# Optimization experiments

Measured on AMD Instinct MI355X. Metric: run time of the kernel, lower is better.

The kernel has to match this reference:

```python
import jax, jax.numpy as jnp
import numpy as np

B, S, E, H = 8, 1024, 1024, 16
D = E // H          # head_dim = 64
FF = 4 * E          # mlp hidden = 4096
EPS = 1e-5


def setup_inputs() -> dict:
    key = jax.random.key(0)
    ks = jax.random.split(key, 12)
    s_e = 1.0 / np.sqrt(E)
    s_ff = 1.0 / np.sqrt(FF)
    return {
        "x": jax.random.normal(ks[0], (B, S, E), jnp.float32),
        # per-head q/k/v projections stacked: [H, E, D] (math layout: y = x @ W + b)
        "Wq": jax.random.normal(ks[1], (H, E, D), jnp.float32) * s_e,
        "bq": jnp.zeros((H, D), jnp.float32),
        "Wk": jax.random.normal(ks[2], (H, E, D), jnp.float32) * s_e,
        "bk": jnp.zeros((H, D), jnp.float32),
        "Wv": jax.random.normal(ks[3], (H, E, D), jnp.float32) * s_e,
        "bv": jnp.zeros((H, D), jnp.float32),
        # output projection [E, E]
        "Wo": jax.random.normal(ks[4], (E, E), jnp.float32) * s_e,
        "bo": jnp.zeros((E,), jnp.float32),
        # layernorms
        "g1": jnp.ones((E,), jnp.float32),
        "beta1": jnp.zeros((E,), jnp.float32),
        "g2": jnp.ones((E,), jnp.float32),
        "beta2": jnp.zeros((E,), jnp.float32),
        # MLP
        "W1": jax.random.normal(ks[5], (E, FF), jnp.float32) * s_e,
        "c1": jnp.zeros((FF,), jnp.float32),
        "W2": jax.random.normal(ks[6], (FF, E), jnp.float32) * s_ff,
        "c2": jnp.zeros((E,), jnp.float32),
    }


def _layernorm(x, g, b):
    mu = jnp.mean(x, axis=-1, keepdims=True)
    var = jnp.mean(jnp.square(x - mu), axis=-1, keepdims=True)
    return (x - mu) * jax.lax.rsqrt(var + EPS) * g + b


def _block(x, Wq, bq, Wk, bk, Wv, bv, Wo, bo, g1, beta1, g2, beta2, W1, c1, W2, c2):
    # --- attention sublayer (pre-norm) ---
    xn = _layernorm(x, g1, beta1)
    # all heads at once (equivalent to the per-head Python loop)
    q = jnp.einsum("bse,hed->bhsd", xn, Wq) + bq[:, None, :]
    k = jnp.einsum("bse,hed->bhsd", xn, Wk) + bk[:, None, :]
    v = jnp.einsum("bse,hed->bhsd", xn, Wv) + bv[:, None, :]
    scale = D ** -0.5
    scores = jnp.einsum("bhsd,bhtd->bhst", q, k) * scale  # [B,H,S,S]
    w = jax.nn.softmax(scores, axis=-1)
    ctx = jnp.einsum("bhst,bhtd->bhsd", w, v)             # [B,H,S,D]
    ctx = ctx.transpose(0, 2, 1, 3).reshape(x.shape[0], x.shape[1], E)  # concat heads
    attn_out = ctx @ Wo + bo
    x = x + attn_out
    # --- MLP sublayer (pre-norm) ---
    xn = _layernorm(x, g2, beta2)
    h = jax.nn.gelu(xn @ W1 + c1, approximate=False)
    return x + (h @ W2 + c2)


def reference(x, Wq, bq, Wk, bk, Wv, bv, Wo, bo, g1, beta1, g2, beta2, W1, c1, W2, c2):
    return _block(x, Wq, bq, Wk, bk, Wv, bv, Wo, bo, g1, beta1, g2, beta2, W1, c1, W2, c2)
```

## Files before the change

kernel.cpp:

```cpp
#include <hip/hip_runtime.h>
#include <math.h>


typedef _Float16 h16;
typedef __attribute__((ext_vector_type(8))) _Float16 f16x8;
typedef __attribute__((ext_vector_type(4))) float f32x4;

__device__ __forceinline__ void gl2lds16(const void* g, void* l) {
  __builtin_amdgcn_global_load_lds(
      (const __attribute__((address_space(1))) void*)g,
      (__attribute__((address_space(3))) void*)l, 16, 0, 0);
}

__global__ __launch_bounds__(256) void repack_kernel(
    const float* __restrict__ Wq, const float* __restrict__ Wk,
    const float* __restrict__ Wv, const float* __restrict__ Wo,
    const float* __restrict__ W1, const float* __restrict__ W2,
    const float* __restrict__ bq, const float* __restrict__ bk,
    const float* __restrict__ bv,
    h16* __restrict__ WqkvT, h16* __restrict__ WoT, h16* __restrict__ W1T,
    h16* __restrict__ W2T, float* __restrict__ bqkv)
{
  const int t = blockIdx.x;
  const int tid = threadIdx.x;
  if (t == 3072) {
    for (int i = tid; i < 3072; i += 256)
      bqkv[i] = (i < 1024) ? bq[i] : (i < 2048 ? bk[i - 1024] : bv[i - 2048]);
    return;
  }
  __shared__ float ld[64 * 65];

  const float* src; h16* dst;
  int sRS, dRS, k0, sn0, dn0;
  if (t < 768) {
    const int m = t >> 8, tt = t & 255, h = tt >> 4, tk = tt & 15;
    src = ((m == 0) ? Wq : (m == 1) ? Wk : Wv) + (size_t)h * 65536;
    dst = WqkvT; sRS = 64; dRS = 1024;
    k0 = tk * 64; sn0 = 0; dn0 = m * 1024 + h * 64;
  } else if (t < 1024) {
    const int tt = t - 768, tk = tt >> 4, tn = tt & 15;
    src = Wo; dst = WoT; sRS = 1024; dRS = 1024;
    k0 = tk * 64; sn0 = tn * 64; dn0 = tn * 64;
  } else if (t < 2048) {
    const int tt = t - 1024, tk = tt >> 6, tn = tt & 63;
    src = W1; dst = W1T; sRS = 4096; dRS = 1024;
    k0 = tk * 64; sn0 = tn * 64; dn0 = tn * 64;
  } else {
    const int tt = t - 2048, tk = tt >> 4, tn = tt & 15;
    src = W2; dst = W2T; sRS = 1024; dRS = 4096;
    k0 = tk * 64; sn0 = tn * 64; dn0 = tn * 64;
  }

  #pragma unroll
  for (int p = 0; p < 16; ++p) {
    const int idx = p * 256 + tid;
    const int r = idx >> 6, c = idx & 63;
    ld[c * 65 + r] = src[(size_t)(k0 + r) * sRS + sn0 + c];
  }
  __syncthreads();
  #pragma unroll
  for (int p = 0; p < 8; ++p) {
    const int idx = p * 512 + tid * 2;
    const int n = idx >> 6, k = idx & 63;
    union { unsigned int u; h16 e[2]; } pk;
    pk.e[0] = (h16)ld[n * 65 + k];
    pk.e[1] = (h16)ld[n * 65 + k + 1];
    *(unsigned int*)&dst[(size_t)(dn0 + n) * dRS + k0 + k] = pk.u;
  }
}

template <int IT>
__global__ __launch_bounds__(256) void ln_kernel(
    const void* __restrict__ in, const float* __restrict__ gw,
    const float* __restrict__ bw, h16* __restrict__ outp)
{
  const int row = blockIdx.x;
  const int tid = threadIdx.x;
  float v[4];
  if (IT == 0) {
    const float* p = (const float*)in + (size_t)row * 1024 + tid * 4;
    float4 tt = *(const float4*)p;
    v[0] = tt.x; v[1] = tt.y; v[2] = tt.z; v[3] = tt.w;
  } else {
    const h16* p = (const h16*)in + (size_t)row * 1024 + tid * 4;
    union { uint2 u; h16 h[4]; } raw;
    raw.u = *(const uint2*)p;
    v[0] = (float)raw.h[0]; v[1] = (float)raw.h[1];
    v[2] = (float)raw.h[2]; v[3] = (float)raw.h[3];
  }
  float s = v[0] + v[1] + v[2] + v[3];
  float ss = v[0]*v[0] + v[1]*v[1] + v[2]*v[2] + v[3]*v[3];
  #pragma unroll
  for (int off = 32; off >= 1; off >>= 1) {
    s += __shfl_down(s, off);
    ss += __shfl_down(ss, off);
  }
  __shared__ float red[8];
  const int w = tid >> 6;
  if ((tid & 63) == 0) { red[w] = s; red[4 + w] = ss; }
  __syncthreads();
  s = red[0] + red[1] + red[2] + red[3];
  ss = red[4] + red[5] + red[6] + red[7];
  const float mean = s * (1.0f / 1024.0f);
  const float var = ss * (1.0f / 1024.0f) - mean * mean;
  const float inv = rsqrtf(fmaxf(var, 0.0f) + 1e-5f);
  union { uint2 u; h16 h[4]; } pk;
  #pragma unroll
  for (int i = 0; i < 4; ++i)
    pk.h[i] = (h16)((v[i] - mean) * inv * gw[tid * 4 + i] + bw[tid * 4 + i]);
  *(uint2*)(outp + (size_t)row * 1024 + tid * 4) = pk.u;
}

#define GEMM8_LDS 131072

template <int MODE>
__global__ __launch_bounds__(512, 2) void gemm8_bt(
    const h16* __restrict__ A, const h16* __restrict__ BT,
    const float* __restrict__ bias, const void* __restrict__ res,
    void* __restrict__ out, int M, int N, int K)
{
  extern __shared__ __align__(16) char smem[];
  const int tid = threadIdx.x;
  const int lane = tid & 63;
  const int l15 = lane & 15, quad = lane >> 4;
  const int w = tid >> 6;
  const int wr = w >> 2, wc = w & 3;
  const int m0 = blockIdx.y * 256, n0 = blockIdx.x * 256;
  const int NT = K >> 5;

  const int sk = (((tid & 3) ^ ((tid >> 3) & 3)) << 3);
  const h16* gA = A + (size_t)(m0 + (tid >> 2)) * K + sk;
  const h16* gB = BT + (size_t)(n0 + (tid >> 2)) * K + sk;
  const int d0 = tid * 16;

  const int x4 = (quad ^ ((l15 >> 1) & 3)) << 4;
  const int aoff = (wr * 128 + l15) * 64 + x4;
  const int boff = 16384 + (wc * 64 + l15) * 64 + x4;

  f32x4 zero = {0.f, 0.f, 0.f, 0.f};
  f32x4 acc[8][4];
  #pragma unroll
  for (int a = 0; a < 8; ++a)
    #pragma unroll
    for (int b = 0; b < 4; ++b) acc[a][b] = zero;

  #pragma unroll
  for (int tt = 0; tt < 3; ++tt) {
    char* bp = smem + tt * 32768;
    gl2lds16(gA + (size_t)tt * 32, bp + d0);
    gl2lds16(gA + (size_t)tt * 32 + (size_t)128 * K, bp + 8192 + d0);
    gl2lds16(gB + (size_t)tt * 32, bp + 16384 + d0);
    gl2lds16(gB + (size_t)tt * 32 + (size_t)128 * K, bp + 24576 + d0);
  }
  asm volatile("s_waitcnt vmcnt(8)" ::: "memory");
  __builtin_amdgcn_sched_barrier(0);
  __builtin_amdgcn_s_barrier();

  for (int t = 0; t < NT; ++t) {
    const char* Tb = smem + (t & 3) * 32768;
    char* Pb = smem + ((t + 3) & 3) * 32768;
    const bool pf = (t + 3) < NT;
    f16x8 bf[4], af[4], af2[4];

    #pragma unroll
    for (int ni = 0; ni < 4; ++ni)
      bf[ni] = *(const f16x8*)(Tb + boff + ni * 1024);
    #pragma unroll
    for (int mi = 0; mi < 4; ++mi)
      af[mi] = *(const f16x8*)(Tb + aoff + mi * 1024);
    if (pf) {
      const h16* g = gA + (size_t)(t + 3) * 32;
      gl2lds16(g, Pb + d0);
      gl2lds16(g + (size_t)128 * K, Pb + 8192 + d0);
    }
    __builtin_amdgcn_s_barrier();
    __builtin_amdgcn_s_setprio(1);
    #pragma unroll
    for (int mi = 0; mi < 4; ++mi)
      #pragma unroll
      for (int ni = 0; ni < 4; ++ni)
        acc[mi][ni] = __builtin_amdgcn_mfma_f32_16x16x32_f16(af[mi], bf[ni], acc[mi][ni], 0, 0, 0);
    __builtin_amdgcn_s_setprio(0);

    #pragma unroll
    for (int mi = 0; mi < 4; ++mi)
      af2[mi] = *(const f16x8*)(Tb + aoff + (mi + 4) * 1024);
    if (pf) {
      const h16* g = gB + (size_t)(t + 3) * 32;
      gl2lds16(g, Pb + 16384 + d0);
      gl2lds16(g + (size_t)128 * K, Pb + 24576 + d0);
    }
    __builtin_amdgcn_s_barrier();
    __builtin_amdgcn_s_setprio(1);
    #pragma unroll
    for (int mi = 0; mi < 4; ++mi)
      #pragma unroll
      for (int ni = 0; ni < 4; ++ni)
        acc[mi + 4][ni] = __builtin_amdgcn_mfma_f32_16x16x32_f16(af2[mi], bf[ni], acc[mi + 4][ni], 0, 0, 0);
    __builtin_amdgcn_s_setprio(0);

    if (pf) {
      asm volatile("s_waitcnt vmcnt(8)" ::: "memory");
    } else if (t + 3 == NT) {
      asm volatile("s_waitcnt vmcnt(4)" ::: "memory");
    } else if (t + 2 == NT) {
      asm volatile("s_waitcnt vmcnt(0)" ::: "memory");
    }
    __builtin_amdgcn_sched_barrier(0);
    __builtin_amdgcn_s_barrier();
  }

  #pragma unroll
  for (int mi = 0; mi < 8; ++mi) {
    #pragma unroll
    for (int ni = 0; ni < 4; ++ni) {
      #pragma unroll
      for (int i = 0; i < 4; ++i) {
        const int r = m0 + wr * 128 + mi * 16 + quad * 4 + i;
        const int c = n0 + wc * 64 + ni * 16 + l15;
        const size_t idx = (size_t)r * N + c;
        float v = acc[mi][ni][i] + bias[c];
        if (MODE == 0) {
          ((h16*)out)[idx] = (h16)v;
        } else if (MODE == 1) {
          v += ((const float*)res)[idx];
          ((h16*)out)[idx] = (h16)v;
        } else if (MODE == 2) {
          const float e = __expf(v * (-1.5957691216f - 0.0713548163f * v * v));
          v = v / (1.0f + e);
          ((h16*)out)[idx] = (h16)v;
        } else {
          v += (float)((const h16*)res)[idx];
          ((float*)out)[idx] = v;
        }
      }
    }
  }
}

#define GEMM_LDS 147456

template <int MODE>
__global__ __launch_bounds__(512, 2) void gemm_bt(
    const h16* __restrict__ A, const h16* __restrict__ BT,
    const float* __restrict__ bias, const void* __restrict__ res,
    void* __restrict__ out, int M, int N, int K)
{
  extern __shared__ __align__(16) char smem[];
  const int tid = threadIdx.x;
  const int lane = tid & 63, w = tid >> 6;
  const int l15 = lane & 15, quad = lane >> 4;
  const int wm = w >> 1, wn = w & 1;
  const int m0 = blockIdx.y * 256, n0 = blockIdx.x * 128;
  const int NT = K >> 6;

  const int srow = w * 8 + (lane >> 3);
  const int scol = ((lane & 7) ^ ((lane >> 3) & 7)) * 8;
  const h16* gA = A + (size_t)(m0 + srow) * K + scol;
  const h16* gB = BT + (size_t)(n0 + srow) * K + scol;
  const int ldsw = w * 1024;

  const int arow = wm * 64 + l15;
  const int brow = wn * 64 + l15;
  const int x7 = l15 & 7;
  const int sw0 = (quad ^ x7) << 4;
  const int sw1 = ((4 | quad) ^ x7) << 4;

  f32x4 zero = {0.f, 0.f, 0.f, 0.f};
  f32x4 acc[4][4];
  #pragma unroll
  for (int a = 0; a < 4; ++a)
    #pragma unroll
    for (int b = 0; b < 4; ++b) acc[a][b] = zero;

  {
    char* b0 = smem;
    char* b1 = smem + 49152;
    #pragma unroll
    for (int j = 0; j < 4; ++j) gl2lds16(gA + (size_t)j * 64 * K, b0 + j * 8192 + ldsw);
    #pragma unroll
    for (int j = 0; j < 2; ++j) gl2lds16(gB + (size_t)j * 64 * K, b0 + 32768 + j * 8192 + ldsw);
    #pragma unroll
    for (int j = 0; j < 4; ++j) gl2lds16(gA + 64 + (size_t)j * 64 * K, b1 + j * 8192 + ldsw);
    #pragma unroll
    for (int j = 0; j < 2; ++j) gl2lds16(gB + 64 + (size_t)j * 64 * K, b1 + 32768 + j * 8192 + ldsw);
  }
  asm volatile("s_waitcnt vmcnt(6)" ::: "memory");
  __builtin_amdgcn_sched_barrier(0);
  __builtin_amdgcn_s_barrier();

  int cur = 0, pre = 2;
  for (int t = 0; t < NT; ++t) {
    const char* Ab = smem + cur * 49152;
    const char* Bb = Ab + 32768;
    char* Pb = smem + pre * 49152;
    const bool pf = (t + 2) < NT;
    f16x8 af[4], bf[4][2];

    #pragma unroll
    for (int mi = 0; mi < 4; ++mi) {
      af[mi] = *(const f16x8*)(Ab + (arow + mi * 16) * 128 + sw0);
    }
    f16x8 af1[4];
    #pragma unroll
    for (int mi = 0; mi < 4; ++mi)
      af1[mi] = *(const f16x8*)(Ab + (arow + mi * 16) * 128 + sw1);
    #pragma unroll
    for (int ni = 0; ni < 2; ++ni) {
      bf[ni][0] = *(const f16x8*)(Bb + (brow + ni * 16) * 128 + sw0);
      bf[ni][1] = *(const f16x8*)(Bb + (brow + ni * 16) * 128 + sw1);
    }
    if (pf) {
      const h16* g = gA + (size_t)(t + 2) * 64;
      #pragma unroll
      for (int j = 0; j < 4; ++j) gl2lds16(g + (size_t)j * 64 * K, Pb + j * 8192 + ldsw);
    }
    __builtin_amdgcn_s_barrier();
    __builtin_amdgcn_s_setprio(1);
    #pragma unroll
    for (int mi = 0; mi < 4; ++mi)
      #pragma unroll
      for (int ni = 0; ni < 2; ++ni) {
        acc[mi][ni] = __builtin_amdgcn_mfma_f32_16x16x32_f16(af[mi], bf[ni][0], acc[mi][ni], 0, 0, 0);
        acc[mi][ni] = __builtin_amdgcn_mfma_f32_16x16x32_f16(af1[mi], bf[ni][1], acc[mi][ni], 0, 0, 0);
      }
    __builtin_amdgcn_s_setprio(0);
    __builtin_amdgcn_s_barrier();

    #pragma unroll
    for (int ni = 2; ni < 4; ++ni) {
      bf[ni][0] = *(const f16x8*)(Bb + (brow + ni * 16) * 128 + sw0);
      bf[ni][1] = *(const f16x8*)(Bb + (brow + ni * 16) * 128 + sw1);
    }
    if (pf) {
      const h16* g = gB + (size_t)(t + 2) * 64;
      #pragma unroll
      for (int j = 0; j < 2; ++j) gl2lds16(g + (size_t)j * 64 * K, Pb + 32768 + j * 8192 + ldsw);
    }
    __builtin_amdgcn_s_barrier();
    __builtin_amdgcn_s_setprio(1);
    #pragma unroll
    for (int mi = 0; mi < 4; ++mi)
      #pragma unroll
      for (int ni = 2; ni < 4; ++ni) {
        acc[mi][ni] = __builtin_amdgcn_mfma_f32_16x16x32_f16(af[mi], bf[ni][0], acc[mi][ni], 0, 0, 0);
        acc[mi][ni] = __builtin_amdgcn_mfma_f32_16x16x32_f16(af1[mi], bf[ni][1], acc[mi][ni], 0, 0, 0);
      }
    __builtin_amdgcn_s_setprio(0);
    if (pf) {
      asm volatile("s_waitcnt vmcnt(6)" ::: "memory");
    } else if (t + 2 == NT) {
      asm volatile("s_waitcnt vmcnt(0)" ::: "memory");
    }
    __builtin_amdgcn_sched_barrier(0);
    __builtin_amdgcn_s_barrier();
    cur = (cur == 2) ? 0 : cur + 1;
    pre = (pre == 2) ? 0 : pre + 1;
  }

  #pragma unroll
  for (int mi = 0; mi < 4; ++mi) {
    #pragma unroll
    for (int ni = 0; ni < 4; ++ni) {
      #pragma unroll
      for (int i = 0; i < 4; ++i) {
        const int r = m0 + wm * 64 + mi * 16 + quad * 4 + i;
        const int c = n0 + wn * 64 + ni * 16 + l15;
        const size_t idx = (size_t)r * N + c;
        float v = acc[mi][ni][i] + bias[c];
        if (MODE == 0) {
          ((h16*)out)[idx] = (h16)v;
        } else if (MODE == 1) {
          v += ((const float*)res)[idx];
          ((h16*)out)[idx] = (h16)v;
        } else if (MODE == 2) {
          const float e = __expf(v * (-1.5957691216f - 0.0713548163f * v * v));
          v = v / (1.0f + e);
          ((h16*)out)[idx] = (h16)v;
        } else {
          v += (float)((const h16*)res)[idx];
          ((float*)out)[idx] = v;
        }
      }
    }
  }
}

__global__ __launch_bounds__(256, 2) void attn_kernel(
    const h16* __restrict__ qkv, h16* __restrict__ ctx)
{
  const int qb = blockIdx.x;
  const int bh = blockIdx.y;
  const int b = bh >> 4, h = bh & 15;
  const int tid = threadIdx.x;
  const int w = tid >> 6, lane = tid & 63;
  const int l15 = lane & 15, quad = lane >> 4;

  __shared__ __align__(16) h16 Ks[64 * 80];
  __shared__ __align__(16) h16 Vt[64 * 80];
  __shared__ __align__(16) h16 Ps[256 * 80];

  const size_t qrow0 = (size_t)(b * 1024 + qb * 256);
  for (int c = tid; c < 2048; c += 256) {
    const int row = c >> 3, kc = (c & 7) * 8;
    uint4 raw = *(const uint4*)(qkv + (qrow0 + row) * 3072 + h * 64 + kc);
    union { uint4 v; h16 e[8]; } in4, out4;
    in4.v = raw;
    #pragma unroll
    for (int i = 0; i < 8; ++i) out4.e[i] = in4.e[i] * (h16)0.125f;
    *(uint4*)&Ps[row * 80 + kc] = out4.v;
  }
  __syncthreads();
  f16x8 aq[4][2];
  #pragma unroll
  for (int r = 0; r < 4; ++r)
    #pragma unroll
    for (int s = 0; s < 2; ++s)
      aq[r][s] = *(const f16x8*)&Ps[(w * 64 + r * 16 + l15) * 80 + s * 32 + quad * 8];

  f32x4 zero = {0.f, 0.f, 0.f, 0.f};
  f32x4 o_acc[4][4];
  float l_p[4][4];
  #pragma unroll
  for (int r = 0; r < 4; ++r)
    #pragma unroll
    for (int i = 0; i < 4; ++i) { o_acc[r][i] = zero; l_p[r][i] = 0.f; }

  h16* Pw = &Ps[w * 64 * 80];

  for (int jt = 0; jt < 16; ++jt) {
    __syncthreads();
    const size_t kv0 = (size_t)(b * 1024 + jt * 64);
    for (int c = tid; c < 512; c += 256) {
      const int row = c >> 3, kc = (c & 7) * 8;
      *(uint4*)&Ks[row * 80 + kc] =
          *(const uint4*)(qkv + (kv0 + row) * 3072 + 1024 + h * 64 + kc);
    }
    #pragma unroll
    for (int cc = 0; cc < 2; ++cc) {
      const int d0 = (w + cc * 4) * 8;
      uint4 raw = *(const uint4*)(qkv + (kv0 + lane) * 3072 + 2048 + h * 64 + d0);
      union { uint4 v; h16 e[8]; } in4;
      in4.v = raw;
      #pragma unroll
      for (int i = 0; i < 8; ++i) Vt[(d0 + i) * 80 + lane] = in4.e[i];
    }
    __syncthreads();

    f16x8 kf[4][2];
    #pragma unroll
    for (int ni = 0; ni < 4; ++ni)
      #pragma unroll
      for (int s = 0; s < 2; ++s)
        kf[ni][s] = *(const f16x8*)&Ks[(ni * 16 + l15) * 80 + s * 32 + quad * 8];
    #pragma unroll
    for (int r = 0; r < 4; ++r) {
      f32x4 s_acc[4];
      #pragma unroll
      for (int i = 0; i < 4; ++i) s_acc[i] = zero;
      #pragma unroll
      for (int ni = 0; ni < 4; ++ni)
        #pragma unroll
        for (int s = 0; s < 2; ++s)
          s_acc[ni] = __builtin_amdgcn_mfma_f32_16x16x32_f16(aq[r][s], kf[ni][s], s_acc[ni], 0, 0, 0);
      #pragma unroll
      for (int ni = 0; ni < 4; ++ni)
        #pragma unroll
        for (int i = 0; i < 4; ++i) {
          float p = __expf(s_acc[ni][i]);
          l_p[r][i] += p;
          Pw[(r * 16 + quad * 4 + i) * 80 + ni * 16 + l15] = (h16)p;
        }
    }

    f16x8 vf[4][2];
    #pragma unroll
    for (int ni = 0; ni < 4; ++ni)
      #pragma unroll
      for (int s = 0; s < 2; ++s)
        vf[ni][s] = *(const f16x8*)&Vt[(ni * 16 + l15) * 80 + s * 32 + quad * 8];
    #pragma unroll
    for (int r = 0; r < 4; ++r) {
      f16x8 ap0 = *(const f16x8*)&Pw[(r * 16 + l15) * 80 + quad * 8];
      f16x8 ap1 = *(const f16x8*)&Pw[(r * 16 + l15) * 80 + 32 + quad * 8];
      #pragma unroll
      for (int ni = 0; ni < 4; ++ni) {
        o_acc[r][ni] = __builtin_amdgcn_mfma_f32_16x16x32_f16(ap0, vf[ni][0], o_acc[r][ni], 0, 0, 0);
        o_acc[r][ni] = __builtin_amdgcn_mfma_f32_16x16x32_f16(ap1, vf[ni][1], o_acc[r][ni], 0, 0, 0);
      }
    }
  }

  #pragma unroll
  for (int r = 0; r < 4; ++r)
    #pragma unroll
    for (int i = 0; i < 4; ++i) {
      float lt = l_p[r][i];
      #pragma unroll
      for (int off = 1; off < 16; off <<= 1) lt += __shfl_xor(lt, off);
      const float rinv = 1.0f / lt;
      const size_t row = qrow0 + w * 64 + r * 16 + quad * 4 + i;
      #pragma unroll
      for (int ni = 0; ni < 4; ++ni)
        ctx[row * 1024 + h * 64 + ni * 16 + l15] = (h16)(o_acc[r][ni][i] * rinv);
    }
}

extern "C" void kernel_launch(void* const* d_in, const int* in_sizes, int n_in,
                              void* d_out, int out_size, void* d_ws, size_t ws_size,
                              hipStream_t stream) {
  const float* x   = (const float*)d_in[0];
  const float* Wq  = (const float*)d_in[1];
  const float* bq  = (const float*)d_in[2];
  const float* Wk  = (const float*)d_in[3];
  const float* bk  = (const float*)d_in[4];
  const float* Wv  = (const float*)d_in[5];
  const float* bv  = (const float*)d_in[6];
  const float* Wo  = (const float*)d_in[7];
  const float* bo  = (const float*)d_in[8];
  const float* g1  = (const float*)d_in[9];
  const float* be1 = (const float*)d_in[10];
  const float* g2  = (const float*)d_in[11];
  const float* be2 = (const float*)d_in[12];
  const float* W1  = (const float*)d_in[13];
  const float* c1  = (const float*)d_in[14];
  const float* W2  = (const float*)d_in[15];
  const float* c2  = (const float*)d_in[16];

  char* ws = (char*)d_ws;
  h16*   WqkvT = (h16*)(ws + 0);
  h16*   WoT   = (h16*)(ws + 6291456);
  h16*   W1T   = (h16*)(ws + 8388608);
  h16*   W2T   = (h16*)(ws + 16777216);
  float* bqkv  = (float*)(ws + 25165824);
  h16*   bufA  = (h16*)(ws + 25178112);
  h16*   qkv   = (h16*)(ws + 41955328);
  h16*   x1    = (h16*)(ws + 41955328);
  h16*   hbuf  = (h16*)(ws + 58732544);

  static bool attr_done = false;
  if (!attr_done) {
    hipFuncSetAttribute((const void*)gemm_bt<1>, hipFuncAttributeMaxDynamicSharedMemorySize, GEMM_LDS);
    hipFuncSetAttribute((const void*)gemm_bt<3>, hipFuncAttributeMaxDynamicSharedMemorySize, GEMM_LDS);
    hipFuncSetAttribute((const void*)gemm8_bt<0>, hipFuncAttributeMaxDynamicSharedMemorySize, GEMM8_LDS);
    hipFuncSetAttribute((const void*)gemm8_bt<2>, hipFuncAttributeMaxDynamicSharedMemorySize, GEMM8_LDS);
    attr_done = true;
  }

  repack_kernel<<<dim3(3073), dim3(256), 0, stream>>>(Wq, Wk, Wv, Wo, W1, W2, bq, bk, bv,
                                                      WqkvT, WoT, W1T, W2T, bqkv);
  ln_kernel<0><<<dim3(8192), dim3(256), 0, stream>>>(x, g1, be1, bufA);
  gemm8_bt<0><<<dim3(12, 32), dim3(512), GEMM8_LDS, stream>>>(bufA, WqkvT, bqkv, nullptr, qkv,
                                                              8192, 3072, 1024);
  attn_kernel<<<dim3(4, 128), dim3(256), 0, stream>>>(qkv, bufA);
  gemm_bt<1><<<dim3(8, 32), dim3(512), GEMM_LDS, stream>>>(bufA, WoT, bo, x, x1,
                                                           8192, 1024, 1024);
  ln_kernel<1><<<dim3(8192), dim3(256), 0, stream>>>(x1, g2, be2, bufA);
  gemm8_bt<2><<<dim3(16, 32), dim3(512), GEMM8_LDS, stream>>>(bufA, W1T, c1, nullptr, hbuf,
                                                              8192, 4096, 1024);
  gemm_bt<3><<<dim3(8, 32), dim3(512), GEMM_LDS, stream>>>(hbuf, W2T, c2, x1, d_out,
                                                           8192, 1024, 4096);
}
```

Measured before the change: 506.8 us.

## Rewrite 256x256 GEMM mainloop as double-buffered K=64 ping-pong with quadrant MFMA phases

Replaces the 4-stage K=32 pipeline in the QKV and W1 GEMMs with two 64 KB LDS buffers holding K=64 tiles, an 8-way XOR swizzle, and a hand-scheduled loop. Each K=64 tile is processed in four quadrant MFMA phases. Each phase is wrapped in barriers and interleaved with partial global-to-LDS stages of the next tile. The aim is to keep LDS reads and global prefetch hidden behind MFMA work and to reduce per-iteration waitcnt and barrier overhead per K element. In exchange there are more barriers per tile, shallower prefetch depth, and reliance on exact vmcnt counts that must be correct.

```diff
diff --git a/kernel.cpp b/kernel.cpp
--- a/kernel.cpp
+++ b/kernel.cpp
@@ -111,31 +111,34 @@
   *(uint2*)(outp + (size_t)row * 1024 + tid * 4) = pk.u;
 }
 
-#define GEMM8_LDS 131072
+#define GEMM201_LDS 131072
 
 template <int MODE>
-__global__ __launch_bounds__(512, 2) void gemm8_bt(
+__global__ __launch_bounds__(512, 2) void gemm201(
     const h16* __restrict__ A, const h16* __restrict__ BT,
     const float* __restrict__ bias, const void* __restrict__ res,
     void* __restrict__ out, int M, int N, int K)
 {
   extern __shared__ __align__(16) char smem[];
   const int tid = threadIdx.x;
-  const int lane = tid & 63;
+  const int lane = tid & 63, w = tid >> 6;
   const int l15 = lane & 15, quad = lane >> 4;
-  const int w = tid >> 6;
   const int wr = w >> 2, wc = w & 3;
   const int m0 = blockIdx.y * 256, n0 = blockIdx.x * 256;
-  const int NT = K >> 5;
-
-  const int sk = (((tid & 3) ^ ((tid >> 3) & 3)) << 3);
-  const h16* gA = A + (size_t)(m0 + (tid >> 2)) * K + sk;
-  const h16* gB = BT + (size_t)(n0 + (tid >> 2)) * K + sk;
-  const int d0 = tid * 16;
-
-  const int x4 = (quad ^ ((l15 >> 1) & 3)) << 4;
-  const int aoff = (wr * 128 + l15) * 64 + x4;
-  const int boff = 16384 + (wc * 64 + l15) * 64 + x4;
+  const int NI = K >> 7;
+
+  const int sr = tid >> 3;
+  const int sk = ((tid & 7) ^ (sr & 7)) * 8;
+  const h16* gAs = A + (size_t)(m0 + sr) * K + sk;
+  const h16* gBs = BT + (size_t)(n0 + sr) * K + sk;
+  const int dst0 = tid * 16;
+
+  const int x7 = l15 & 7;
+  const int sw0 = (quad ^ x7) << 4;
+  const int sw1 = ((4 + quad) ^ x7) << 4;
+  const int aBase = wr * 16384;
+  const int bBase = 32768 + (wc >> 1) * 16384;
+  const int bRow0 = (wc & 1) * 64;
 
   f32x4 zero = {0.f, 0.f, 0.f, 0.f};
   f32x4 acc[8][4];
@@ -144,70 +147,99 @@
     #pragma unroll
     for (int b = 0; b < 4; ++b) acc[a][b] = zero;
 
-  #pragma unroll
-  for (int tt = 0; tt < 3; ++tt) {
-    char* bp = smem + tt * 32768;
-    gl2lds16(gA + (size_t)tt * 32, bp + d0);
-    gl2lds16(gA + (size_t)tt * 32 + (size_t)128 * K, bp + 8192 + d0);
-    gl2lds16(gB + (size_t)tt * 32, bp + 16384 + d0);
-    gl2lds16(gB + (size_t)tt * 32 + (size_t)128 * K, bp + 24576 + d0);
-  }
-  asm volatile("s_waitcnt vmcnt(8)" ::: "memory");
-  __builtin_amdgcn_sched_barrier(0);
-  __builtin_amdgcn_s_barrier();
-
-  for (int t = 0; t < NT; ++t) {
-    const char* Tb = smem + (t & 3) * 32768;
-    char* Pb = smem + ((t + 3) & 3) * 32768;
-    const bool pf = (t + 3) < NT;
-    f16x8 bf[4], af[4], af2[4];
-
-    #pragma unroll
-    for (int ni = 0; ni < 4; ++ni)
-      bf[ni] = *(const f16x8*)(Tb + boff + ni * 1024);
+  f16x8 AF0[4][2], AF1[4][2], BF0[2][2], BF1[2][2];
+
+  auto rdA = [&](int bufo, int mi0, f16x8 (&AF)[4][2]) {
+    #pragma unroll
+    for (int mi = 0; mi < 4; ++mi) {
+      const char* p = smem + bufo + aBase + ((mi0 + mi) * 16 + l15) * 128;
+      AF[mi][0] = *(const f16x8*)(p + sw0);
+      AF[mi][1] = *(const f16x8*)(p + sw1);
+    }
+  };
+  auto rdB = [&](int bufo, int ni0, f16x8 (&BF)[2][2]) {
+    #pragma unroll
+    for (int ni = 0; ni < 2; ++ni) {
+      const char* p = smem + bufo + bBase + (bRow0 + (ni0 + ni) * 16 + l15) * 128;
+      BF[ni][0] = *(const f16x8*)(p + sw0);
+      BF[ni][1] = *(const f16x8*)(p + sw1);
+    }
+  };
+  auto mmq = [&](int mi0, int ni0, f16x8 (&AF)[4][2], f16x8 (&BF)[2][2]) {
+    __builtin_amdgcn_s_setprio(1);
     #pragma unroll
     for (int mi = 0; mi < 4; ++mi)
-      af[mi] = *(const f16x8*)(Tb + aoff + mi * 1024);
-    if (pf) {
-      const h16* g = gA + (size_t)(t + 3) * 32;
-      gl2lds16(g, Pb + d0);
-      gl2lds16(g + (size_t)128 * K, Pb + 8192 + d0);
-    }
-    __builtin_amdgcn_s_barrier();
-    __builtin_amdgcn_s_setprio(1);
-    #pragma unroll
-    for (int mi = 0; mi < 4; ++mi)
-      #pragma unroll
-      for (int ni = 0; ni < 4; ++ni)
-        acc[mi][ni] = __builtin_amdgcn_mfma_f32_16x16x32_f16(af[mi], bf[ni], acc[mi][ni], 0, 0, 0);
+      #pragma unroll
+      for (int ni = 0; ni < 2; ++ni) {
+        acc[mi0 + mi][ni0 + ni] = __builtin_amdgcn_mfma_f32_16x16x32_f16(
+            AF[mi][0], BF[ni][0], acc[mi0 + mi][ni0 + ni], 0, 0, 0);
+        acc[mi0 + mi][ni0 + ni] = __builtin_amdgcn_mfma_f32_16x16x32_f16(
+            AF[mi][1], BF[ni][1], acc[mi0 + mi][ni0 + ni], 0, 0, 0);
+      }
     __builtin_amdgcn_s_setprio(0);
-
-    #pragma unroll
-    for (int mi = 0; mi < 4; ++mi)
-      af2[mi] = *(const f16x8*)(Tb + aoff + (mi + 4) * 1024);
-    if (pf) {
-      const h16* g = gB + (size_t)(t + 3) * 32;
-      gl2lds16(g, Pb + 16384 + d0);
-      gl2lds16(g + (size_t)128 * K, Pb + 24576 + d0);
-    }
-    __builtin_amdgcn_s_barrier();
-    __builtin_amdgcn_s_setprio(1);
-    #pragma unroll
-    for (int mi = 0; mi < 4; ++mi)
-      #pragma unroll
-      for (int ni = 0; ni < 4; ++ni)
-        acc[mi + 4][ni] = __builtin_amdgcn_mfma_f32_16x16x32_f16(af2[mi], bf[ni], acc[mi + 4][ni], 0, 0, 0);
-    __builtin_amdgcn_s_setprio(0);
-
-    if (pf) {
-      asm volatile("s_waitcnt vmcnt(8)" ::: "memory");
-    } else if (t + 3 == NT) {
-      asm volatile("s_waitcnt vmcnt(4)" ::: "memory");
-    } else if (t + 2 == NT) {
-      asm volatile("s_waitcnt vmcnt(0)" ::: "memory");
-    }
-    __builtin_amdgcn_sched_barrier(0);
-    __builtin_amdgcn_s_barrier();
+  };
+
+#define STG_A(b, h, T) { \
+    char* d_ = smem + (b) * 65536 + (h) * 16384 + dst0; \
+    const h16* g_ = gAs + (size_t)((h) * 128) * K + (size_t)(T) * 64; \
+    gl2lds16(g_, d_); gl2lds16(g_ + (size_t)64 * K, d_ + 8192); }
+#define STG_B(b, h, T) { \
+    char* d_ = smem + (b) * 65536 + 32768 + (h) * 16384 + dst0; \
+    const h16* g_ = gBs + (size_t)((h) * 128) * K + (size_t)(T) * 64; \
+    gl2lds16(g_, d_); gl2lds16(g_ + (size_t)64 * K, d_ + 8192); }
+#define BAR __builtin_amdgcn_s_barrier()
+#define VMC(n) { asm volatile("s_waitcnt vmcnt(" #n ")" ::: "memory"); \
+                 __builtin_amdgcn_sched_barrier(0); }
+
+  STG_A(0, 0, 0); STG_A(0, 1, 0); STG_B(0, 0, 0); STG_B(0, 1, 0);
+  STG_A(1, 0, 1); STG_A(1, 1, 1); STG_B(1, 0, 1);
+  VMC(6);
+  BAR;
+
+  for (int i = 0; i < NI - 1; ++i) {
+    const int E = 2 * i, O = E + 1;
+    rdA(0, 0, AF0); rdB(0, 0, BF0);
+    STG_B(1, 1, O);
+    BAR; mmq(0, 0, AF0, BF0); BAR;
+    rdA(0, 4, AF1);
+    BAR; mmq(4, 0, AF1, BF0); BAR;
+    rdB(0, 2, BF1);
+    STG_A(0, 0, E + 2);
+    BAR; mmq(4, 2, AF1, BF1); BAR;
+    STG_A(0, 1, E + 2); STG_B(0, 0, E + 2);
+    VMC(6);
+    BAR; mmq(0, 2, AF0, BF1); BAR;
+    rdA(65536, 0, AF0); rdB(65536, 0, BF0);
+    STG_B(0, 1, E + 2);
+    BAR; mmq(0, 0, AF0, BF0); BAR;
+    rdA(65536, 4, AF1);
+    BAR; mmq(4, 0, AF1, BF0); BAR;
+    rdB(65536, 2, BF1);
+    STG_A(1, 0, O + 2);
+    BAR; mmq(4, 2, AF1, BF1); BAR;
+    STG_A(1, 1, O + 2); STG_B(1, 0, O + 2);
+    VMC(6);
+    BAR; mmq(0, 2, AF0, BF1); BAR;
+  }
+
+  {
+    const int O = 2 * NI - 1;
+    rdA(0, 0, AF0); rdB(0, 0, BF0);
+    STG_B(1, 1, O);
+    BAR; mmq(0, 0, AF0, BF0); BAR;
+    rdA(0, 4, AF1);
+    BAR; mmq(4, 0, AF1, BF0); BAR;
+    rdB(0, 2, BF1);
+    BAR; mmq(4, 2, AF1, BF1); BAR;
+    VMC(0);
+    BAR; mmq(0, 2, AF0, BF1); BAR;
+    rdA(65536, 0, AF0); rdB(65536, 0, BF0);
+    BAR; mmq(0, 0, AF0, BF0); BAR;
+    rdA(65536, 4, AF1);
+    BAR; mmq(4, 0, AF1, BF0); BAR;
+    rdB(65536, 2, BF1);
+    BAR; mmq(4, 2, AF1, BF1); BAR;
+    mmq(0, 2, AF0, BF1);
   }
 
   #pragma unroll
@@ -236,6 +268,10 @@
       }
     }
   }
+#undef STG_A
+#undef STG_B
+#undef BAR
+#undef VMC
 }
 
 #define GEMM_LDS 147456
@@ -295,13 +331,11 @@
     const char* Bb = Ab + 32768;
     char* Pb = smem + pre * 49152;
     const bool pf = (t + 2) < NT;
-    f16x8 af[4], bf[4][2];
-
-    #pragma unroll
-    for (int mi = 0; mi < 4; ++mi) {
+    f16x8 af[4], af1[4], bf[4][2];
+
+    #pragma unroll
+    for (int mi = 0; mi < 4; ++mi)
       af[mi] = *(const f16x8*)(Ab + (arow + mi * 16) * 128 + sw0);
-    }
-    f16x8 af1[4];
     #pragma unroll
     for (int mi = 0; mi < 4; ++mi)
       af1[mi] = *(const f16x8*)(Ab + (arow + mi * 16) * 128 + sw1);
@@ -542,22 +576,22 @@
   if (!attr_done) {
     hipFuncSetAttribute((const void*)gemm_bt<1>, hipFuncAttributeMaxDynamicSharedMemorySize, GEMM_LDS);
     hipFuncSetAttribute((const void*)gemm_bt<3>, hipFuncAttributeMaxDynamicSharedMemorySize, GEMM_LDS);
-    hipFuncSetAttribute((const void*)gemm8_bt<0>, hipFuncAttributeMaxDynamicSharedMemorySize, GEMM8_LDS);
-    hipFuncSetAttribute((const void*)gemm8_bt<2>, hipFuncAttributeMaxDynamicSharedMemorySize, GEMM8_LDS);
+    hipFuncSetAttribute((const void*)gemm201<0>, hipFuncAttributeMaxDynamicSharedMemorySize, GEMM201_LDS);
+    hipFuncSetAttribute((const void*)gemm201<2>, hipFuncAttributeMaxDynamicSharedMemorySize, GEMM201_LDS);
     attr_done = true;
   }
 
   repack_kernel<<<dim3(3073), dim3(256), 0, stream>>>(Wq, Wk, Wv, Wo, W1, W2, bq, bk, bv,
                                                       WqkvT, WoT, W1T, W2T, bqkv);
   ln_kernel<0><<<dim3(8192), dim3(256), 0, stream>>>(x, g1, be1, bufA);
-  gemm8_bt<0><<<dim3(12, 32), dim3(512), GEMM8_LDS, stream>>>(bufA, WqkvT, bqkv, nullptr, qkv,
-                                                              8192, 3072, 1024);
+  gemm201<0><<<dim3(12, 32), dim3(512), GEMM201_LDS, stream>>>(bufA, WqkvT, bqkv, nullptr, qkv,
+                                                               8192, 3072, 1024);
   attn_kernel<<<dim3(4, 128), dim3(256), 0, stream>>>(qkv, bufA);
   gemm_bt<1><<<dim3(8, 32), dim3(512), GEMM_LDS, stream>>>(bufA, WoT, bo, x, x1,
                                                            8192, 1024, 1024);
   ln_kernel<1><<<dim3(8192), dim3(256), 0, stream>>>(x1, g2, be2, bufA);
-  gemm8_bt<2><<<dim3(16, 32), dim3(512), GEMM8_LDS, stream>>>(bufA, W1T, c1, nullptr, hbuf,
-                                                              8192, 4096, 1024);
+  gemm201<2><<<dim3(16, 32), dim3(512), GEMM201_LDS, stream>>>(bufA, W1T, c1, nullptr, hbuf,
+                                                               8192, 4096, 1024);
   gemm_bt<3><<<dim3(8, 32), dim3(512), GEMM_LDS, stream>>>(hbuf, W2T, c2, x1, d_out,
                                                            8192, 1024, 4096);
 }
```

After: 482.9 us. 1.05x faster.
